# Performance work log

Measured on AMD Instinct MI355X. Metric: run time of the kernel, lower is better.

## Reference

```python
import jax, jax.numpy as jnp
import numpy as np
import math

B, T, C = 4, 2048, 1024
N_HEAD = 16
HEAD = C // N_HEAD  # 64
ROPE_BASE = 10000.0


def rotate_half(x):
    x1, x2 = x[..., : x.shape[-1] // 2], x[..., x.shape[-1] // 2:]
    return jnp.concatenate((-x2, x1), axis=-1)


def rope_cos_sin(seq_len, dim, dtype=jnp.float32):
    inv_freq = 1.0 / (ROPE_BASE ** (jnp.arange(0, dim, 2, dtype=jnp.float32) / dim))
    t = jnp.arange(seq_len, dtype=jnp.float32)
    freqs = jnp.einsum('i,j->ij', t, inv_freq)          # [T, dim/2]
    emb = jnp.concatenate((freqs, freqs), axis=-1)       # [T, dim]
    return jnp.cos(emb).astype(dtype), jnp.sin(emb).astype(dtype)


def setup_inputs() -> dict:
    key = jax.random.key(0)
    ks = jax.random.split(key, 5)
    s_in = 1.0 / math.sqrt(C)
    return {
        'x': jax.random.normal(ks[0], (B, T, C), dtype=jnp.float32),
        'W_qkv': jax.random.normal(ks[1], (C, 3 * C), dtype=jnp.float32) * s_in,
        'b_qkv': jnp.zeros((3 * C,), dtype=jnp.float32),
        'W_proj': jax.random.normal(ks[2], (C, C), dtype=jnp.float32) * s_in,
        'b_proj': jnp.zeros((C,), dtype=jnp.float32),
    }


def reference(x, W_qkv, b_qkv, W_proj, b_proj):
    b, t, c = x.shape
    qkv = x @ W_qkv + b_qkv                               # [B,T,3C]
    q, k, v = jnp.split(qkv, 3, axis=-1)
    # [B,T,C] -> [B,H,T,hd]
    def to_heads(u):
        return u.reshape(b, t, N_HEAD, HEAD).transpose(0, 2, 1, 3)
    q, k, v = to_heads(q), to_heads(k), to_heads(v)
    # RoPE
    cos, sin = rope_cos_sin(t, HEAD, x.dtype)             # [T,hd]
    cos = cos[None, None]; sin = sin[None, None]
    q = q * cos + rotate_half(q) * sin
    k = k * cos + rotate_half(k) * sin
    # naive causal attention (materializes [B,H,T,T] like the original)
    att = jnp.einsum('bhqd,bhkd->bhqk', q, k) * (1.0 / math.sqrt(HEAD))
    causal = jnp.tril(jnp.ones((t, t), dtype=bool))
    att = jnp.where(causal[None, None], att, -jnp.inf)
    att = jax.nn.softmax(att, axis=-1)
    y = jnp.einsum('bhqk,bhkd->bhqd', att, v)             # [B,H,T,hd]
    y = y.transpose(0, 2, 1, 3).reshape(b, t, c)
    return y @ W_proj + b_proj
```

## Files before the change

### kernel.cpp

```cpp
#include <hip/hip_runtime.h>
#include <stdint.h>

#define B_  4
#define T_  2048
#define C_  1024
#define NH_ 16
#define HD_ 64
#define BH_ (B_*NH_)
#define M_  (B_*T_)

using f32x4  = __attribute__((ext_vector_type(4))) float;
using f32x16 = __attribute__((ext_vector_type(16))) float;
using bf16x8 = __attribute__((ext_vector_type(8))) short;

__device__ __forceinline__ unsigned short f2bf(float x) {
  union { float f; uint32_t u; } v; v.f = x;
  uint32_t u = v.u;
  return (unsigned short)((u + 0x7FFFu + ((u >> 16) & 1u)) >> 16);
}

__device__ __forceinline__ uint32_t cvtpk(float a, float b) {
  uint32_t r;
  asm("v_cvt_pk_bf16_f32 %0, %1, %2" : "=v"(r) : "v"(a), "v"(b));
  return r;
}

__device__ __forceinline__ void gload16(const void* g, void* l) {
  __builtin_amdgcn_global_load_lds(
      (const __attribute__((address_space(1))) void*)g,
      (__attribute__((address_space(3))) void*)l, 16, 0, 0);
}

#define BAR() do { asm volatile("" ::: "memory"); __builtin_amdgcn_s_barrier(); \
                   asm volatile("" ::: "memory"); } while (0)
#define VMC(N) asm volatile("s_waitcnt vmcnt(" #N ")" ::: "memory")

__global__ __launch_bounds__(256)
void k_prep(const float* __restrict__ x,      unsigned short* __restrict__ xb,
            const float* __restrict__ Wqkv,   unsigned short* __restrict__ WqkvT,
            const float* __restrict__ Wproj,  unsigned short* __restrict__ WprojT,
            float* __restrict__ cosT, float* __restrict__ sinT) {
  __shared__ float tile[32][33];
  const int blk = blockIdx.x;
  const int tid = threadIdx.x;
  if (blk < 8192) {
    int i = (blk * 256 + tid) * 4;
    float4 v = *(const float4*)(x + i);
    ushort4 o;
    o.x = f2bf(v.x); o.y = f2bf(v.y); o.z = f2bf(v.z); o.w = f2bf(v.w);
    *(ushort4*)(xb + i) = o;
    return;
  }
  const int tx = tid & 31, ty = tid >> 5;
  if (blk < 12288) {
    const float* W; unsigned short* WT; int N, local;
    if (blk < 11264) { W = Wqkv;  WT = WqkvT;  N = 3*C_; local = blk - 8192; }
    else             { W = Wproj; WT = WprojT; N = C_;   local = blk - 11264; }
    const int NT = N / 32;
    const int bx = local % NT, by = local / NT;
    #pragma unroll
    for (int i = 0; i < 32; i += 8)
      tile[ty + i][tx] = W[(size_t)(by*32 + ty + i) * N + bx*32 + tx];
    __syncthreads();
    #pragma unroll
    for (int i = 0; i < 32; i += 8)
      WT[(size_t)(bx*32 + ty + i) * C_ + by*32 + tx] = f2bf(tile[tx][ty + i]);
    return;
  }
  {
    int t = (blk - 12288) * 8 + ty;
    float inv = expf(-(float)tx * (9.210340371976184f / 32.0f));
    float f = (float)t * inv;
    cosT[t*32 + tx] = cosf(f);
    sinT[t*32 + tx] = sinf(f);
  }
}

template<int N, int K, int EPI>
__global__ __launch_bounds__(256)
void k_gemm(const unsigned short* __restrict__ Ag,
            const unsigned short* __restrict__ BT,
            const float* __restrict__ bias,
            const float* __restrict__ cosT,
            const float* __restrict__ sinT,
            unsigned short* __restrict__ Qh,
            unsigned short* __restrict__ Kh,
            unsigned short* __restrict__ VhT,
            float* __restrict__ outF) {
  __shared__ alignas(16) unsigned short As[2][128*64];
  __shared__ alignas(16) unsigned short Bs[2][128*64];
  const int tid  = threadIdx.x;
  const int lane = tid & 63;
  const int wv   = tid >> 6;
  const int wm   = wv >> 1, wn = wv & 1;
  const int l15  = lane & 15, l4 = lane >> 4;
  const int NT  = N / 128;
  const int id  = ((int)blockIdx.x & 7) * ((int)gridDim.x >> 3) + ((int)blockIdx.x >> 3);
  const int m0  = (id / NT) * 128;
  const int n0  = (id % NT) * 128;

  f32x4 acc[4][4] = {};

  const int g0 = l4 ^ (l15 & 7);
  const int g1 = (4 + l4) ^ (l15 & 7);
  const int rowA = wm*64 + l15, rowB = wn*64 + l15;
  const unsigned short* aRd0k0 = &As[0][rowA*64 + g0*8];
  const unsigned short* aRd0k1 = &As[0][rowA*64 + g1*8];
  const unsigned short* aRd1k0 = &As[1][rowA*64 + g0*8];
  const unsigned short* aRd1k1 = &As[1][rowA*64 + g1*8];
  const unsigned short* bRd0k0 = &Bs[0][rowB*64 + g0*8];
  const unsigned short* bRd0k1 = &Bs[0][rowB*64 + g1*8];
  const unsigned short* bRd1k0 = &Bs[1][rowB*64 + g0*8];
  const unsigned short* bRd1k1 = &Bs[1][rowB*64 + g1*8];

  const int srow = wv*8 + (lane >> 3);
  const int sg   = (lane & 7) ^ ((lane >> 3) & 7);
  const int voff = srow*K + sg*8;
  const int aUni = m0*K, bUni = n0*K;
  const int ldsD = wv*512;

#define STG(BUF, KT) do { \
  const int _u = (KT)*64; \
  _Pragma("unroll") for (int it = 0; it < 4; ++it) { \
    gload16(Ag + (aUni + it*(32*K) + _u) + voff, (void*)(&As[BUF][it*2048 + ldsD])); \
    gload16(BT + (bUni + it*(32*K) + _u) + voff, (void*)(&Bs[BUF][it*2048 + ldsD])); \
  } \
} while (0)

#define CMP(AK0, AK1, BK0, BK1) do { \
  bf16x8 afr[4][2], bfr[4][2]; \
  _Pragma("unroll") for (int mi = 0; mi < 4; ++mi) { \
    afr[mi][0] = *(const bf16x8*)((AK0) + mi*1024); \
    afr[mi][1] = *(const bf16x8*)((AK1) + mi*1024); \
    bfr[mi][0] = *(const bf16x8*)((BK0) + mi*1024); \
    bfr[mi][1] = *(const bf16x8*)((BK1) + mi*1024); \
  } \
  __builtin_amdgcn_s_setprio(1); \
  _Pragma("unroll") for (int ks = 0; ks < 2; ++ks) \
  _Pragma("unroll") for (int mi = 0; mi < 4; ++mi) \
  _Pragma("unroll") for (int ni = 0; ni < 4; ++ni) \
    acc[mi][ni] = __builtin_amdgcn_mfma_f32_16x16x32_bf16( \
        afr[mi][ks], bfr[ni][ks], acc[mi][ni], 0, 0, 0); \
  __builtin_amdgcn_s_setprio(0); \
} while (0)

  STG(0, 0);
  #pragma unroll 1
  for (int i = 0; i < K/128; ++i) {
    STG(1, 2*i + 1);
    VMC(8);
    BAR();
    CMP(aRd0k0, aRd0k1, bRd0k0, bRd0k1);
    BAR();
    if (i + 1 < K/128) {
      STG(0, 2*i + 2);
      VMC(8);
    } else {
      VMC(0);
    }
    BAR();
    CMP(aRd1k0, aRd1k1, bRd1k0, bRd1k1);
    BAR();
  }
#undef STG
#undef CMP

  if (EPI == 0) {
    const int ncol = n0 + wn*64;
    const int part = ncol >> 10;
    const int hid  = (ncol & 1023) >> 6;
    unsigned short* dstQK = (part == 0) ? Qh : Kh;
    #pragma unroll
    for (int mi = 0; mi < 4; ++mi) {
      #pragma unroll
      for (int j = 0; j < 4; ++j) {
        int row = m0 + wm*64 + mi*16 + l4*4 + j;
        int bb = row >> 11, tt = row & 2047;
        if (part < 2) {
          size_t base = ((size_t)((bb*NH_ + hid) * T_ + tt)) * HD_;
          #pragma unroll
          for (int ni = 0; ni < 2; ++ni) {
            int d = ni*16 + l15;
            float a1 = acc[mi][ni][j]     + bias[ncol + d];
            float a2 = acc[mi][ni + 2][j] + bias[ncol + d + 32];
            float cv = cosT[tt*32 + d], sv = sinT[tt*32 + d];
            float o1 = a1*cv - a2*sv;
            float o2 = a2*cv + a1*sv;
            if (part == 0) { o1 *= 0.18033688011112042f; o2 *= 0.18033688011112042f; }
            dstQK[base + d]      = f2bf(o1);
            dstQK[base + d + 32] = f2bf(o2);
          }
        } else {
          #pragma unroll
          for (int ni = 0; ni < 4; ++ni) {
            int d = ni*16 + l15;
            float av = acc[mi][ni][j] + bias[ncol + d];
            VhT[((size_t)((bb*NH_ + hid) * HD_ + d)) * T_ + tt] = f2bf(av);
          }
        }
      }
    }
  } else {
    #pragma unroll
    for (int mi = 0; mi < 4; ++mi)
      #pragma unroll
      for (int ni = 0; ni < 4; ++ni)
        #pragma unroll
        for (int j = 0; j < 4; ++j) {
          int row = m0 + wm*64 + mi*16 + l4*4 + j;
          int col = n0 + wn*64 + ni*16 + l15;
          outF[(size_t)row * N + col] = acc[mi][ni][j] + bias[col];
        }
  }
}

__global__ __launch_bounds__(256, 3)
void k_attn(const unsigned short* __restrict__ Qh,
            const unsigned short* __restrict__ Kh,
            const unsigned short* __restrict__ VhT,
            unsigned short* __restrict__ Y) {
  __shared__ alignas(16) unsigned short Ks[2][64*64];
  __shared__ alignas(16) unsigned short Vs[2][64*64];
  const int tid  = threadIdx.x;
  const int lane = tid & 63;
  const int wv   = tid >> 6;
  const int l31  = lane & 31;
  const int h    = lane >> 5;
  const int bh   = blockIdx.x & 63;
  const int qb   = 15 - (blockIdx.x >> 6);
  const int r32  = qb*128 + wv*32;
  const int nt   = 2*qb + 2;
  const int qg   = r32 + l31;

  bf16x8 qf[4];
  #pragma unroll
  for (int i = 0; i < 4; ++i)
    qf[i] = *(const bf16x8*)(Qh + ((size_t)(bh*T_ + qg))*HD_ + i*16 + h*8);

  float m_r = -1e30f, l_r = 0.f;
  f32x16 o[2] = {};

  auto stage = [&](int buf, int jt) {
    #pragma unroll
    for (int it = 0; it < 2; ++it) {
      int idx = it*256 + wv*64 + lane;
      int row = idx >> 3, slot = idx & 7;
      int g   = slot ^ (row & 7);
      gload16(Kh  + ((size_t)(bh*T_ + jt*64 + row))*HD_ + g*8,
              (void*)(Ks[buf] + (it*256 + wv*64)*8));
      gload16(VhT + ((size_t)(bh*HD_ + row))*T_ + jt*64 + g*8,
              (void*)(Vs[buf] + (it*256 + wv*64)*8));
    }
  };

  stage(0, 0);
  int cur = 0;

  for (int jt = 0; jt < nt; ++jt) {
    if (jt + 1 < nt) {
      stage(cur ^ 1, jt + 1);
      VMC(4);
    } else {
      VMC(0);
    }
    BAR();

    if (jt*64 <= r32 + 31) {
      f32x16 s[2] = {f32x16{0}, f32x16{0}};
      __builtin_amdgcn_s_setprio(1);
      #pragma unroll
      for (int kb = 0; kb < 2; ++kb)
        #pragma unroll
        for (int i = 0; i < 4; ++i) {
          int r = kb*32 + l31;
          int g = (2*i + h) ^ (r & 7);
          bf16x8 kf = *(const bf16x8*)(Ks[cur] + r*64 + g*8);
          s[kb] = __builtin_amdgcn_mfma_f32_32x32x16_bf16(kf, qf[i], s[kb], 0, 0, 0);
        }
      __builtin_amdgcn_s_setprio(0);

      float p[2][16];
      const bool diag = (jt + 1)*64 > r32;
      #pragma unroll
      for (int kb = 0; kb < 2; ++kb)
        #pragma unroll
        for (int r = 0; r < 16; ++r) {
          float v = s[kb][r];
          if (diag) {
            int key = jt*64 + kb*32 + (r & 3) + 8*(r >> 2) + 4*h;
            v = (key > qg) ? -1e30f : v;
          }
          p[kb][r] = v;
        }

      float mx[16];
      #pragma unroll
      for (int r = 0; r < 16; ++r) mx[r] = fmaxf(p[0][r], p[1][r]);
      #pragma unroll
      for (int st = 8; st > 0; st >>= 1)
        #pragma unroll
        for (int r = 0; r < 8; ++r)
          if (r < st) mx[r] = fmaxf(mx[r], mx[r + st]);
      float tm = fmaxf(mx[0], __shfl_xor(mx[0], 32));

      if (!__all(tm <= m_r + 8.0f)) {
        float mn = fmaxf(m_r, tm);
        float scale = exp2f(m_r - mn);
        m_r = mn;
        l_r *= scale;
        #pragma unroll
        for (int dblk = 0; dblk < 2; ++dblk)
          #pragma unroll
          for (int r = 0; r < 16; ++r)
            o[dblk][r] *= scale;
      }

      #pragma unroll
      for (int kb = 0; kb < 2; ++kb)
        #pragma unroll
        for (int r = 0; r < 16; ++r)
          p[kb][r] = exp2f(p[kb][r] - m_r);

      float sm[16];
      #pragma unroll
      for (int r = 0; r < 16; ++r) sm[r] = p[0][r] + p[1][r];
      #pragma unroll
      for (int st = 8; st > 0; st >>= 1)
        #pragma unroll
        for (int r = 0; r < 8; ++r)
          if (r < st) sm[r] += sm[r + st];
      l_r += sm[0] + __shfl_xor(sm[0], 32);

      #pragma unroll
      for (int kb = 0; kb < 2; ++kb) {
        uint32_t a01 = cvtpk(p[kb][0],  p[kb][1]);
        uint32_t a23 = cvtpk(p[kb][2],  p[kb][3]);
        uint32_t a45 = cvtpk(p[kb][4],  p[kb][5]);
        uint32_t a67 = cvtpk(p[kb][6],  p[kb][7]);
        uint32_t b01 = cvtpk(p[kb][8],  p[kb][9]);
        uint32_t b23 = cvtpk(p[kb][10], p[kb][11]);
        uint32_t b45 = cvtpk(p[kb][12], p[kb][13]);
        uint32_t b67 = cvtpk(p[kb][14], p[kb][15]);
        uint32_t s1 = h ? a01 : a45, s2 = h ? a23 : a67;
        uint32_t s3 = h ? b01 : b45, s4 = h ? b23 : b67;
        uint32_t x1 = __shfl_xor(s1, 32), x2 = __shfl_xor(s2, 32);
        uint32_t x3 = __shfl_xor(s3, 32), x4 = __shfl_xor(s4, 32);
        union { bf16x8 v; uint32_t d[4]; } f0, f1;
        f0.d[0] = h ? x1 : a01;  f0.d[1] = h ? x2 : a23;
        f0.d[2] = h ? a45 : x1;  f0.d[3] = h ? a67 : x2;
        f1.d[0] = h ? x3 : b01;  f1.d[1] = h ? x4 : b23;
        f1.d[2] = h ? b45 : x3;  f1.d[3] = h ? b67 : x4;

        __builtin_amdgcn_s_setprio(1);
        #pragma unroll
        for (int koff = 0; koff < 2; ++koff) {
          bf16x8 pf = koff ? f1.v : f0.v;
          #pragma unroll
          for (int dblk = 0; dblk < 2; ++dblk) {
            int rv = dblk*32 + l31;
            int gv = (kb*4 + koff*2 + h) ^ (rv & 7);
            bf16x8 vf = *(const bf16x8*)(Vs[cur] + rv*64 + gv*8);
            o[dblk] = __builtin_amdgcn_mfma_f32_32x32x16_bf16(vf, pf, o[dblk], 0, 0, 0);
          }
        }
        __builtin_amdgcn_s_setprio(0);
      }
    }

    BAR();
    cur ^= 1;
  }

  int b = bh >> 4, hd = bh & 15;
  float rinv = 1.0f / l_r;
  unsigned short* yrow = Y + ((size_t)(b*T_ + r32 + l31))*C_ + hd*64;
  #pragma unroll
  for (int dblk = 0; dblk < 2; ++dblk)
    #pragma unroll
    for (int g2 = 0; g2 < 4; ++g2) {
      ushort4 o4;
      o4.x = f2bf(o[dblk][g2*4 + 0] * rinv);
      o4.y = f2bf(o[dblk][g2*4 + 1] * rinv);
      o4.z = f2bf(o[dblk][g2*4 + 2] * rinv);
      o4.w = f2bf(o[dblk][g2*4 + 3] * rinv);
      *(ushort4*)(yrow + dblk*32 + g2*8 + 4*h) = o4;
    }
}


extern "C" void kernel_launch(void* const* d_in, const int* in_sizes, int n_in,
                              void* d_out, int out_size, void* d_ws, size_t ws_size,
                              hipStream_t stream) {
  const float* x      = (const float*)d_in[0];
  const float* W_qkv  = (const float*)d_in[1];
  const float* b_qkv  = (const float*)d_in[2];
  const float* W_proj = (const float*)d_in[3];
  const float* b_proj = (const float*)d_in[4];
  float* out = (float*)d_out;

  char* ws = (char*)d_ws;
  size_t off = 0;
  auto alloc = [&](size_t bytes) {
    void* p = ws + off; off += (bytes + 255) & ~(size_t)255; return p;
  };
  unsigned short* xb     = (unsigned short*)alloc((size_t)M_ * C_ * 2);
  unsigned short* WqkvT  = (unsigned short*)alloc((size_t)3 * C_ * C_ * 2);
  unsigned short* WprojT = (unsigned short*)alloc((size_t)C_ * C_ * 2);
  unsigned short* Qh     = (unsigned short*)alloc((size_t)M_ * C_ * 2);
  unsigned short* Kh     = (unsigned short*)alloc((size_t)M_ * C_ * 2);
  unsigned short* VhT    = (unsigned short*)alloc((size_t)M_ * C_ * 2);
  float* cosT = (float*)alloc((size_t)T_ * 32 * 4);
  float* sinT = (float*)alloc((size_t)T_ * 32 * 4);
  unsigned short* Y = xb;

  k_prep<<<dim3(12544), 256, 0, stream>>>(x, xb, W_qkv, WqkvT, W_proj, WprojT,
                                          cosT, sinT);

  k_gemm<3*C_, C_, 0><<<dim3(1536), 256, 0, stream>>>(
      xb, WqkvT, b_qkv, cosT, sinT, Qh, Kh, VhT, nullptr);

  k_attn<<<dim3(T_/128 * BH_), 256, 0, stream>>>(Qh, Kh, VhT, Y);

  k_gemm<C_, C_, 1><<<dim3(512), 256, 0, stream>>>(
      Y, WprojT, b_proj, nullptr, nullptr, nullptr, nullptr, nullptr, out);
}
```

Before: 194.6 us.

## Replace 128x128 GEMM with 256x256-tile 8-wave kernel using interleaved staging

Both GEMMs now use a 512-thread, 8-wave kernel with 256x256 output tiles. Each wave computes a 128x64 sub-tile in four quadrant steps, and global-to-LDS loads for the next K tiles are interleaved between the MFMA phases. The larger tile raises arithmetic intensity and cuts global traffic per FLOP. In exchange, LDS use grows to 128KB per block, so occupancy drops, and the projection GEMM launches only 128 blocks, which may underfill the 256 CUs.

After: 249.5 us. 1.28x slower.

```diff
diff --git a/kernel.cpp b/kernel.cpp
--- a/kernel.cpp
+++ b/kernel.cpp
@@ -8,6 +8,7 @@
 #define HD_ 64
 #define BH_ (B_*NH_)
 #define M_  (B_*T_)
+#define KT_ 16
 
 using f32x4  = __attribute__((ext_vector_type(4))) float;
 using f32x16 = __attribute__((ext_vector_type(16))) float;
@@ -77,140 +78,177 @@
 }
 
 template<int N, int K, int EPI>
-__global__ __launch_bounds__(256)
-void k_gemm(const unsigned short* __restrict__ Ag,
-            const unsigned short* __restrict__ BT,
-            const float* __restrict__ bias,
-            const float* __restrict__ cosT,
-            const float* __restrict__ sinT,
-            unsigned short* __restrict__ Qh,
-            unsigned short* __restrict__ Kh,
-            unsigned short* __restrict__ VhT,
-            float* __restrict__ outF) {
-  __shared__ alignas(16) unsigned short As[2][128*64];
-  __shared__ alignas(16) unsigned short Bs[2][128*64];
+__global__ __launch_bounds__(512)
+void k_gemm8(const unsigned short* __restrict__ Ag,
+             const unsigned short* __restrict__ BT,
+             const float* __restrict__ bias,
+             const float* __restrict__ cosT,
+             const float* __restrict__ sinT,
+             unsigned short* __restrict__ Qh,
+             unsigned short* __restrict__ Kh,
+             unsigned short* __restrict__ VhT,
+             float* __restrict__ outF) {
+  __shared__ alignas(16) unsigned short Asf[2*2*8192];
+  __shared__ alignas(16) unsigned short Bsf[2*2*8192];
   const int tid  = threadIdx.x;
   const int lane = tid & 63;
   const int wv   = tid >> 6;
-  const int wm   = wv >> 1, wn = wv & 1;
+  const int wr   = wv >> 2, wc = wv & 3;
   const int l15  = lane & 15, l4 = lane >> 4;
-  const int NT  = N / 128;
   const int id  = ((int)blockIdx.x & 7) * ((int)gridDim.x >> 3) + ((int)blockIdx.x >> 3);
-  const int m0  = (id / NT) * 128;
-  const int n0  = (id % NT) * 128;
-
-  f32x4 acc[4][4] = {};
+  const int m0  = (id % 32) * 256;
+  const int n0  = (id / 32) * 256;
+
+  f32x4  acc[2][2][4][2] = {};
+  bf16x8 af[4][2], bq0[2][2], bq1[2][2];
 
   const int g0 = l4 ^ (l15 & 7);
   const int g1 = (4 + l4) ^ (l15 & 7);
-  const int rowA = wm*64 + l15, rowB = wn*64 + l15;
-  const unsigned short* aRd0k0 = &As[0][rowA*64 + g0*8];
-  const unsigned short* aRd0k1 = &As[0][rowA*64 + g1*8];
-  const unsigned short* aRd1k0 = &As[1][rowA*64 + g0*8];
-  const unsigned short* aRd1k1 = &As[1][rowA*64 + g1*8];
-  const unsigned short* bRd0k0 = &Bs[0][rowB*64 + g0*8];
-  const unsigned short* bRd0k1 = &Bs[0][rowB*64 + g1*8];
-  const unsigned short* bRd1k0 = &Bs[1][rowB*64 + g0*8];
-  const unsigned short* bRd1k1 = &Bs[1][rowB*64 + g1*8];
-
-  const int srow = wv*8 + (lane >> 3);
-  const int sg   = (lane & 7) ^ ((lane >> 3) & 7);
-  const int voff = srow*K + sg*8;
-  const int aUni = m0*K, bUni = n0*K;
-  const int ldsD = wv*512;
-
-#define STG(BUF, KT) do { \
-  const int _u = (KT)*64; \
-  _Pragma("unroll") for (int it = 0; it < 4; ++it) { \
-    gload16(Ag + (aUni + it*(32*K) + _u) + voff, (void*)(&As[BUF][it*2048 + ldsD])); \
-    gload16(BT + (bUni + it*(32*K) + _u) + voff, (void*)(&Bs[BUF][it*2048 + ldsD])); \
-  } \
-} while (0)
-
-#define CMP(AK0, AK1, BK0, BK1) do { \
-  bf16x8 afr[4][2], bfr[4][2]; \
+  const unsigned short* a0k0 = Asf + (0*2 + wr)*8192 + l15*64 + g0*8;
+  const unsigned short* a0k1 = Asf + (0*2 + wr)*8192 + l15*64 + g1*8;
+  const unsigned short* a1k0 = Asf + (1*2 + wr)*8192 + l15*64 + g0*8;
+  const unsigned short* a1k1 = Asf + (1*2 + wr)*8192 + l15*64 + g1*8;
+  const int bRow = (wc & 1)*64 + l15;
+  const unsigned short* b0k0 = Bsf + (0*2 + (wc>>1))*8192 + bRow*64 + g0*8;
+  const unsigned short* b0k1 = Bsf + (0*2 + (wc>>1))*8192 + bRow*64 + g1*8;
+  const unsigned short* b1k0 = Bsf + (1*2 + (wc>>1))*8192 + bRow*64 + g0*8;
+  const unsigned short* b1k1 = Bsf + (1*2 + (wc>>1))*8192 + bRow*64 + g1*8;
+
+  const int vrow  = tid >> 3;
+  const int vg    = (tid & 7) ^ (vrow & 7);
+  const int vbase = vrow*K + vg*8;
+  const int ldsW  = wv*512;
+
+#define STG_A(BUF, T, HALF) do { \
+  const unsigned short* _s = Ag + (size_t)(m0 + (HALF)*128)*K + (T)*64 + vbase; \
+  unsigned short* _d = Asf + ((BUF)*2 + (HALF))*8192 + ldsW; \
+  gload16(_s, _d); gload16(_s + 64*K, _d + 4096); \
+} while (0)
+
+#define STG_B(BUF, T, HALF) do { \
+  const unsigned short* _s = BT + (size_t)(n0 + (HALF)*128)*K + (T)*64 + vbase; \
+  unsigned short* _d = Bsf + ((BUF)*2 + (HALF))*8192 + ldsW; \
+  gload16(_s, _d); gload16(_s + 64*K, _d + 4096); \
+} while (0)
+
+#define LDA(BUF, QR) do { \
+  const unsigned short* _p0 = (BUF) ? a1k0 : a0k0; \
+  const unsigned short* _p1 = (BUF) ? a1k1 : a0k1; \
   _Pragma("unroll") for (int mi = 0; mi < 4; ++mi) { \
-    afr[mi][0] = *(const bf16x8*)((AK0) + mi*1024); \
-    afr[mi][1] = *(const bf16x8*)((AK1) + mi*1024); \
-    bfr[mi][0] = *(const bf16x8*)((BK0) + mi*1024); \
-    bfr[mi][1] = *(const bf16x8*)((BK1) + mi*1024); \
-  } \
+    af[mi][0] = *(const bf16x8*)(_p0 + (QR)*4096 + mi*1024); \
+    af[mi][1] = *(const bf16x8*)(_p1 + (QR)*4096 + mi*1024); } \
+} while (0)
+
+#define LDB(BUF, QC, BQ) do { \
+  const unsigned short* _p0 = (BUF) ? b1k0 : b0k0; \
+  const unsigned short* _p1 = (BUF) ? b1k1 : b0k1; \
+  _Pragma("unroll") for (int ni = 0; ni < 2; ++ni) { \
+    BQ[ni][0] = *(const bf16x8*)(_p0 + (QC)*2048 + ni*1024); \
+    BQ[ni][1] = *(const bf16x8*)(_p1 + (QC)*2048 + ni*1024); } \
+} while (0)
+
+#define MMQ(QR, QC, BQ) do { \
   __builtin_amdgcn_s_setprio(1); \
   _Pragma("unroll") for (int ks = 0; ks < 2; ++ks) \
   _Pragma("unroll") for (int mi = 0; mi < 4; ++mi) \
-  _Pragma("unroll") for (int ni = 0; ni < 4; ++ni) \
-    acc[mi][ni] = __builtin_amdgcn_mfma_f32_16x16x32_bf16( \
-        afr[mi][ks], bfr[ni][ks], acc[mi][ni], 0, 0, 0); \
+  _Pragma("unroll") for (int ni = 0; ni < 2; ++ni) \
+    acc[QR][QC][mi][ni] = __builtin_amdgcn_mfma_f32_16x16x32_bf16( \
+        af[mi][ks], BQ[ni][ks], acc[QR][QC][mi][ni], 0, 0, 0); \
   __builtin_amdgcn_s_setprio(0); \
 } while (0)
 
-  STG(0, 0);
+#define TILE(BUF, T) do { \
+   \
+  LDA(BUF, 0); LDB(BUF, 0, bq0); \
+  if ((T) + 1 < KT_) STG_A(BUF^1, (T)+1, 1); \
+  BAR(); MMQ(0, 0, bq0); BAR(); \
+   \
+  LDB(BUF, 1, bq1); \
+  BAR(); MMQ(0, 1, bq1); BAR(); \
+   \
+  LDA(BUF, 1); \
+  if ((T) + 2 < KT_) STG_B(BUF, (T)+2, 0); \
+  BAR(); MMQ(1, 0, bq0); BAR(); \
+   \
+  if ((T) + 2 < KT_) { STG_B(BUF, (T)+2, 1); STG_A(BUF, (T)+2, 0); } \
+  BAR(); MMQ(1, 1, bq1); \
+  if ((T) + 2 < KT_)      { VMC(6); } \
+  else if ((T) + 1 < KT_) { VMC(0); } \
+  BAR(); \
+} while (0)
+
+  STG_A(0, 0, 0); STG_A(0, 0, 1); STG_B(0, 0, 0); STG_B(0, 0, 1);
+  STG_B(1, 1, 0); STG_B(1, 1, 1); STG_A(1, 1, 0);
+  VMC(6);
+  BAR();
+
   #pragma unroll 1
-  for (int i = 0; i < K/128; ++i) {
-    STG(1, 2*i + 1);
-    VMC(8);
-    BAR();
-    CMP(aRd0k0, aRd0k1, bRd0k0, bRd0k1);
-    BAR();
-    if (i + 1 < K/128) {
-      STG(0, 2*i + 2);
-      VMC(8);
-    } else {
-      VMC(0);
-    }
-    BAR();
-    CMP(aRd1k0, aRd1k1, bRd1k0, bRd1k1);
-    BAR();
-  }
-#undef STG
-#undef CMP
+  for (int i = 0; i < KT_/2; ++i) {
+    TILE(0, 2*i);
+    TILE(1, 2*i + 1);
+  }
+  VMC(0);
+
+#undef STG_A
+#undef STG_B
+#undef LDA
+#undef LDB
+#undef MMQ
+#undef TILE
 
   if (EPI == 0) {
-    const int ncol = n0 + wn*64;
+    const int ncol = n0 + wc*64;
     const int part = ncol >> 10;
     const int hid  = (ncol & 1023) >> 6;
     unsigned short* dstQK = (part == 0) ? Qh : Kh;
     #pragma unroll
-    for (int mi = 0; mi < 4; ++mi) {
-      #pragma unroll
-      for (int j = 0; j < 4; ++j) {
-        int row = m0 + wm*64 + mi*16 + l4*4 + j;
-        int bb = row >> 11, tt = row & 2047;
-        if (part < 2) {
-          size_t base = ((size_t)((bb*NH_ + hid) * T_ + tt)) * HD_;
-          #pragma unroll
-          for (int ni = 0; ni < 2; ++ni) {
-            int d = ni*16 + l15;
-            float a1 = acc[mi][ni][j]     + bias[ncol + d];
-            float a2 = acc[mi][ni + 2][j] + bias[ncol + d + 32];
-            float cv = cosT[tt*32 + d], sv = sinT[tt*32 + d];
-            float o1 = a1*cv - a2*sv;
-            float o2 = a2*cv + a1*sv;
-            if (part == 0) { o1 *= 0.18033688011112042f; o2 *= 0.18033688011112042f; }
-            dstQK[base + d]      = f2bf(o1);
-            dstQK[base + d + 32] = f2bf(o2);
-          }
-        } else {
-          #pragma unroll
-          for (int ni = 0; ni < 4; ++ni) {
-            int d = ni*16 + l15;
-            float av = acc[mi][ni][j] + bias[ncol + d];
-            VhT[((size_t)((bb*NH_ + hid) * HD_ + d)) * T_ + tt] = f2bf(av);
+    for (int qr = 0; qr < 2; ++qr)
+      #pragma unroll
+      for (int mi = 0; mi < 4; ++mi)
+        #pragma unroll
+        for (int j = 0; j < 4; ++j) {
+          int row = m0 + wr*128 + qr*64 + mi*16 + l4*4 + j;
+          int bb = row >> 11, tt = row & 2047;
+          if (part < 2) {
+            size_t base = ((size_t)((bb*NH_ + hid) * T_ + tt)) * HD_;
+            #pragma unroll
+            for (int ni = 0; ni < 2; ++ni) {
+              int d = ni*16 + l15;
+              float a1 = acc[qr][0][mi][ni][j] + bias[ncol + d];
+              float a2 = acc[qr][1][mi][ni][j] + bias[ncol + d + 32];
+              float cv = cosT[tt*32 + d], sv = sinT[tt*32 + d];
+              float o1 = a1*cv - a2*sv;
+              float o2 = a2*cv + a1*sv;
+              if (part == 0) { o1 *= 0.18033688011112042f; o2 *= 0.18033688011112042f; }
+              dstQK[base + d]      = f2bf(o1);
+              dstQK[base + d + 32] = f2bf(o2);
+            }
+          } else {
+            #pragma unroll
+            for (int qc = 0; qc < 2; ++qc)
+              #pragma unroll
+              for (int ni = 0; ni < 2; ++ni) {
+                int d = qc*32 + ni*16 + l15;
+                float av = acc[qr][qc][mi][ni][j] + bias[ncol + d];
+                VhT[((size_t)((bb*NH_ + hid) * HD_ + d)) * T_ + tt] = f2bf(av);
+              }
           }
         }
-      }
-    }
   } else {
     #pragma unroll
-    for (int mi = 0; mi < 4; ++mi)
-      #pragma unroll
-      for (int ni = 0; ni < 4; ++ni)
-        #pragma unroll
-        for (int j = 0; j < 4; ++j) {
-          int row = m0 + wm*64 + mi*16 + l4*4 + j;
-          int col = n0 + wn*64 + ni*16 + l15;
-          outF[(size_t)row * N + col] = acc[mi][ni][j] + bias[col];
-        }
+    for (int qr = 0; qr < 2; ++qr)
+      #pragma unroll
+      for (int qc = 0; qc < 2; ++qc)
+        #pragma unroll
+        for (int mi = 0; mi < 4; ++mi)
+          #pragma unroll
+          for (int ni = 0; ni < 2; ++ni)
+            #pragma unroll
+            for (int j = 0; j < 4; ++j) {
+              int row = m0 + wr*128 + qr*64 + mi*16 + l4*4 + j;
+              int col = n0 + wc*64 + qc*32 + ni*16 + l15;
+              outF[(size_t)row * N + col] = acc[qr][qc][mi][ni][j] + bias[col];
+            }
   }
 }
 
@@ -416,11 +454,11 @@
   k_prep<<<dim3(12544), 256, 0, stream>>>(x, xb, W_qkv, WqkvT, W_proj, WprojT,
                                           cosT, sinT);
 
-  k_gemm<3*C_, C_, 0><<<dim3(1536), 256, 0, stream>>>(
+  k_gemm8<3*C_, C_, 0><<<dim3(384), 512, 0, stream>>>(
       xb, WqkvT, b_qkv, cosT, sinT, Qh, Kh, VhT, nullptr);
 
   k_attn<<<dim3(T_/128 * BH_), 256, 0, stream>>>(Qh, Kh, VhT, Y);
 
-  k_gemm<C_, C_, 1><<<dim3(512), 256, 0, stream>>>(
+  k_gemm8<C_, C_, 1><<<dim3(128), 512, 0, stream>>>(
       Y, WprojT, b_proj, nullptr, nullptr, nullptr, nullptr, nullptr, out);
 }
```

## Stage attention K/V tiles through registers into padded LDS

Applied to the files above, without the earlier changes.

Replaces the async global-to-LDS loads (gload16 with an XOR swizzle and vmcnt waits) with plain global loads into registers. The loads for the next tile are issued before compute and written to the other LDS buffer after compute, so one barrier per iteration replaces two. The LDS rows are padded to 72 elements instead of swizzled, which simplifies address math for the MFMA operand reads. The cost is extra VGPRs for the staged tile under the 3-waves-per-SIMD launch bound, plus a different LDS bank-conflict pattern from padding.

Result: no change. 193.1 us (-0.7%).

```diff
diff --git a/kernel.cpp b/kernel.cpp
--- a/kernel.cpp
+++ b/kernel.cpp
@@ -214,13 +214,14 @@
   }
 }
 
+#define LDW 72
 __global__ __launch_bounds__(256, 3)
 void k_attn(const unsigned short* __restrict__ Qh,
             const unsigned short* __restrict__ Kh,
             const unsigned short* __restrict__ VhT,
             unsigned short* __restrict__ Y) {
-  __shared__ alignas(16) unsigned short Ks[2][64*64];
-  __shared__ alignas(16) unsigned short Vs[2][64*64];
+  __shared__ alignas(16) unsigned short Ks[2][64*LDW];
+  __shared__ alignas(16) unsigned short Vs[2][64*LDW];
   const int tid  = threadIdx.x;
   const int lane = tid & 63;
   const int wv   = tid >> 6;
@@ -240,41 +241,48 @@
   float m_r = -1e30f, l_r = 0.f;
   f32x16 o[2] = {};
 
-  auto stage = [&](int buf, int jt) {
-    #pragma unroll
-    for (int it = 0; it < 2; ++it) {
-      int idx = it*256 + wv*64 + lane;
-      int row = idx >> 3, slot = idx & 7;
-      int g   = slot ^ (row & 7);
-      gload16(Kh  + ((size_t)(bh*T_ + jt*64 + row))*HD_ + g*8,
-              (void*)(Ks[buf] + (it*256 + wv*64)*8));
-      gload16(VhT + ((size_t)(bh*HD_ + row))*T_ + jt*64 + g*8,
-              (void*)(Vs[buf] + (it*256 + wv*64)*8));
-    }
+  const int srow  = tid >> 3;
+  const int sslot = tid & 7;
+  const unsigned short* kSrc0 = Kh  + ((size_t)(bh*T_ + srow))*HD_ + sslot*8;
+  const unsigned short* kSrc1 = Kh  + ((size_t)(bh*T_ + 32 + srow))*HD_ + sslot*8;
+  const unsigned short* vSrc0 = VhT + ((size_t)(bh*HD_ + srow))*T_ + sslot*8;
+  const unsigned short* vSrc1 = VhT + ((size_t)(bh*HD_ + 32 + srow))*T_ + sslot*8;
+  const int wOff0 = srow*LDW + sslot*8;
+  const int wOff1 = (32 + srow)*LDW + sslot*8;
+
+  uint4 kr0, kr1, vr0, vr1;
+  auto ldg = [&](int jt) {
+    kr0 = *(const uint4*)(kSrc0 + (size_t)jt*64*HD_);
+    kr1 = *(const uint4*)(kSrc1 + (size_t)jt*64*HD_);
+    vr0 = *(const uint4*)(vSrc0 + jt*64);
+    vr1 = *(const uint4*)(vSrc1 + jt*64);
   };
-
-  stage(0, 0);
+  auto wst = [&](int buf) {
+    *(uint4*)(&Ks[buf][wOff0]) = kr0;
+    *(uint4*)(&Ks[buf][wOff1]) = kr1;
+    *(uint4*)(&Vs[buf][wOff0]) = vr0;
+    *(uint4*)(&Vs[buf][wOff1]) = vr1;
+  };
+
+  ldg(0); wst(0);
+  __syncthreads();
   int cur = 0;
 
   for (int jt = 0; jt < nt; ++jt) {
-    if (jt + 1 < nt) {
-      stage(cur ^ 1, jt + 1);
-      VMC(4);
-    } else {
-      VMC(0);
-    }
-    BAR();
+    const bool pf = (jt + 1 < nt);
+    if (pf) ldg(jt + 1);
 
     if (jt*64 <= r32 + 31) {
+      const unsigned short* kb_ = &Ks[cur][l31*LDW + h*8];
+      const unsigned short* vb_ = &Vs[cur][l31*LDW + h*8];
+
       f32x16 s[2] = {f32x16{0}, f32x16{0}};
       __builtin_amdgcn_s_setprio(1);
       #pragma unroll
       for (int kb = 0; kb < 2; ++kb)
         #pragma unroll
         for (int i = 0; i < 4; ++i) {
-          int r = kb*32 + l31;
-          int g = (2*i + h) ^ (r & 7);
-          bf16x8 kf = *(const bf16x8*)(Ks[cur] + r*64 + g*8);
+          bf16x8 kf = *(const bf16x8*)(kb_ + kb*32*LDW + i*16);
           s[kb] = __builtin_amdgcn_mfma_f32_32x32x16_bf16(kf, qf[i], s[kb], 0, 0, 0);
         }
       __builtin_amdgcn_s_setprio(0);
@@ -357,9 +365,7 @@
           bf16x8 pf = koff ? f1.v : f0.v;
           #pragma unroll
           for (int dblk = 0; dblk < 2; ++dblk) {
-            int rv = dblk*32 + l31;
-            int gv = (kb*4 + koff*2 + h) ^ (rv & 7);
-            bf16x8 vf = *(const bf16x8*)(Vs[cur] + rv*64 + gv*8);
+            bf16x8 vf = *(const bf16x8*)(vb_ + dblk*32*LDW + kb*32 + koff*16);
             o[dblk] = __builtin_amdgcn_mfma_f32_32x32x16_bf16(vf, pf, o[dblk], 0, 0, 0);
           }
         }
@@ -367,7 +373,8 @@
       }
     }
 
-    BAR();
+    if (pf) wst(cur ^ 1);
+    __syncthreads();
     cur ^= 1;
   }
 
```
